# Optimization experiments

Hardware: AMD Instinct MI355X
Metric: run time of the kernel (lower is better)

Reference implementation:

```python
import jax, jax.numpy as jnp
import numpy as np


def _kernelize(data, projection_matrix):
    # FAVOR+ positive softmax features: ratio * h(x) * f(x @ P^T)
    # h(x) = exp(-||x||^2 / 2), f(u) = exp(u)
    d = data.shape[-1]
    r = projection_matrix.shape[0]
    data_norm = (d ** -0.25) * data                       # [n, d]
    ratio = r ** -0.5
    data_dash = jnp.einsum('id,rd->ir', data_norm, projection_matrix)  # [n, r]
    h = jnp.exp(-0.5 * jnp.sum(data_norm * data_norm, axis=-1, keepdims=True))  # [n, 1]
    return ratio * h * jnp.exp(data_dash)                 # [n, r]


def setup_inputs() -> dict:
    key = jax.random.key(0)
    k1, k2, k3, k4 = jax.random.split(key, 4)
    n, d, dv, r = 65536, 64, 64, 256
    q = jax.random.normal(k1, (n, d), dtype=jnp.float32)
    k = jax.random.normal(k2, (n, d), dtype=jnp.float32)
    v = jax.random.normal(k3, (n, dv), dtype=jnp.float32)
    projection_matrix = jax.random.normal(k4, (r, d), dtype=jnp.float32)
    return {"q": q, "k": k, "v": v, "projection_matrix": projection_matrix}


def reference(q, k, v, projection_matrix):
    q_hat = _kernelize(q, projection_matrix)              # [n, r]
    k_hat = _kernelize(k, projection_matrix)              # [n, r]
    z = k_hat.T @ v                                       # [r, dv]  (FAVOR associativity)
    w = q_hat @ z                                         # [n, dv]
    d_inv = 1.0 / jnp.sum(q_hat * jnp.sum(k_hat, axis=0), axis=1, keepdims=True)  # [n, 1]
    return d_inv * w
```

## Files before the change

kernel.cpp:

```cpp
#include <hip/hip_runtime.h>
#include <math.h>

typedef __attribute__((ext_vector_type(8))) short bf16x8;
typedef __attribute__((ext_vector_type(4))) float f32x4;

#define RFEAT 256
#define NBKV 512
#define LDK 136
#define PCOL 66
#define PARTU (128 * PCOL)
#define NGRP 8

#define SCLOG2E 0.51006971688f
#define RC_COEF -0.09016844006f
#define LOG2RATIO -4.0f

__device__ __forceinline__ unsigned short f2bf(float f) {
    union { float f; unsigned int u; } v; v.f = f;
    unsigned int r = v.u + 0x7FFFu + ((v.u >> 16) & 1u);
    return (unsigned short)(r >> 16);
}
__device__ __forceinline__ unsigned int pack2bf(float lo, float hi) {
    return (unsigned int)f2bf(lo) | ((unsigned int)f2bf(hi) << 16);
}
__device__ __forceinline__ float bf2f(unsigned int bits16) {
    union { unsigned int u; float f; } v; v.u = bits16 << 16; return v.f;
}

__global__ __launch_bounds__(256)
void prep_pb_kernel(const float* __restrict__ P, unsigned short* __restrict__ Pb)
{
    const int t = threadIdx.x, l = t & 63, g = t >> 6;
    for (int f = g * 8; f < g * 8 + 8; f++) {
        const int kstep = f >> 4, nt = f & 15;
        const float* src = P + (nt * 16 + (l & 15)) * 64 + kstep * 32 + (l >> 4) * 8;
        bf16x8 frag;
        #pragma unroll
        for (int j = 0; j < 8; j++) frag[j] = (short)f2bf(SCLOG2E * src[j]);
        *(bf16x8*)(Pb + f * 512 + l * 8) = frag;
    }
}

__device__ __forceinline__ void phi_chunk8(const float* __restrict__ X, int chunkBase,
                                           const unsigned short* __restrict__ Pb,
                                           unsigned short* phi_lds, float* rc)
{
    const int t = threadIdx.x, l = t & 63, w = t >> 6;
    if (t < 128) {
        const float4* xr = (const float4*)(X + (size_t)(chunkBase + t) * 64);
        float s0 = 0.f, s1 = 0.f;
        #pragma unroll
        for (int j = 0; j < 16; j += 2) {
            float4 a = xr[j];     s0 += a.x*a.x + a.y*a.y + a.z*a.z + a.w*a.w;
            float4 b = xr[j + 1]; s1 += b.x*b.x + b.y*b.y + b.z*b.z + b.w*b.w;
        }
        rc[t] = RC_COEF * (s0 + s1) + LOG2RATIO;
    }
    const float* ar = X + (size_t)(chunkBase + 16 * w + (l & 15)) * 64 + (l >> 4) * 8;
    bf16x8 a0, a1;
    #pragma unroll
    for (int j = 0; j < 8; j++) a0[j] = (short)f2bf(ar[j]);
    #pragma unroll
    for (int j = 0; j < 8; j++) a1[j] = (short)f2bf(ar[32 + j]);
    __syncthreads();
    const float4 rcv = *(const float4*)(rc + 16 * w + 4 * (l >> 4));
    #pragma unroll
    for (int nt = 0; nt < 16; nt++) {
        bf16x8 b0 = *(const bf16x8*)(Pb + nt * 512 + l * 8);
        bf16x8 b1 = *(const bf16x8*)(Pb + (16 + nt) * 512 + l * 8);
        f32x4 acc = (f32x4){rcv.x, rcv.y, rcv.z, rcv.w};
        acc = __builtin_amdgcn_mfma_f32_16x16x32_bf16(a0, b0, acc, 0, 0, 0);
        acc = __builtin_amdgcn_mfma_f32_16x16x32_bf16(a1, b1, acc, 0, 0, 0);
        float p0 = __builtin_amdgcn_exp2f(acc[0]);
        float p1 = __builtin_amdgcn_exp2f(acc[1]);
        float p2 = __builtin_amdgcn_exp2f(acc[2]);
        float p3 = __builtin_amdgcn_exp2f(acc[3]);
        const int col = nt * 16 + (l & 15);
        unsigned int w0 = pack2bf(p0, p1);
        unsigned int w1 = pack2bf(p2, p3);
        unsigned int* dst = (unsigned int*)(phi_lds + col * LDK + 16 * w + 4 * (l >> 4));
        dst[0] = w0;
        dst[1] = w1;
    }
    __syncthreads();
}

__global__ __launch_bounds__(512, 4)
void kv_kernel(const float* __restrict__ Kp, const float* __restrict__ V,
               const unsigned short* __restrict__ Pb, unsigned int* __restrict__ partials)
{
    __shared__ __align__(16) unsigned short phi_lds[RFEAT * LDK];
    __shared__ __align__(16) float rc[128];
    const int t = threadIdx.x, l = t & 63, w = t >> 6;

    f32x4 acc[2][5];
    #pragma unroll
    for (int mt = 0; mt < 2; mt++)
        #pragma unroll
        for (int nt = 0; nt < 5; nt++) acc[mt][nt] = (f32x4){0.f, 0.f, 0.f, 0.f};

    bf16x8 ones;
    #pragma unroll
    for (int j = 0; j < 8; j++) ones[j] = (short)(((l & 15) == 0) ? 0x3F80 : 0);

    const int cb = blockIdx.x * 128;
    phi_chunk8(Kp, cb, Pb, phi_lds, rc);

    #pragma unroll
    for (int ks = 0; ks < 4; ks++) {
        bf16x8 af[2];
        #pragma unroll
        for (int mt = 0; mt < 2; mt++)
            af[mt] = *(const bf16x8*)(phi_lds + (32 * w + mt * 16 + (l & 15)) * LDK
                                      + ks * 32 + (l >> 4) * 8);
        const float* vbase = V + (size_t)(cb + ks * 32 + (l >> 4) * 8) * 64 + (l & 15);
        bf16x8 bf4[4];
        #pragma unroll
        for (int nt = 0; nt < 4; nt++) {
            const float* vp = vbase + nt * 16;
            bf16x8 bb;
            #pragma unroll
            for (int j = 0; j < 8; j++) bb[j] = (short)f2bf(vp[j * 64]);
            bf4[nt] = bb;
        }
        #pragma unroll
        for (int mt = 0; mt < 2; mt++) {
            #pragma unroll
            for (int nt = 0; nt < 4; nt++)
                acc[mt][nt] = __builtin_amdgcn_mfma_f32_16x16x32_bf16(af[mt], bf4[nt], acc[mt][nt], 0, 0, 0);
            acc[mt][4] = __builtin_amdgcn_mfma_f32_16x16x32_bf16(af[mt], ones, acc[mt][4], 0, 0, 0);
        }
    }
    unsigned int* slot = partials + (size_t)blockIdx.x * PARTU;
    #pragma unroll
    for (int mt = 0; mt < 2; mt++) {
        const int fpb = 16 * w + mt * 8 + ((l >> 4) << 1);
        #pragma unroll
        for (int nt = 0; nt < 5; nt++) {
            if (nt == 4 && (l & 15) != 0) continue;
            const int col = nt * 16 + (l & 15);
            slot[fpb * PCOL + col]       = pack2bf(acc[mt][nt][0], acc[mt][nt][1]);
            slot[(fpb + 1) * PCOL + col] = pack2bf(acc[mt][nt][2], acc[mt][nt][3]);
        }
    }
}

__global__ __launch_bounds__(256)
void reduceA_kernel(const unsigned int* __restrict__ partials, float2* __restrict__ p2)
{
    const int idx = blockIdx.x * 256 + threadIdx.x;
    const int g = blockIdx.y;
    const unsigned int* base = partials + (size_t)g * 64 * PARTU + idx;
    float lo0 = 0.f, hi0 = 0.f, lo1 = 0.f, hi1 = 0.f;
    #pragma unroll 4
    for (int s = 0; s < 64; s += 2) {
        unsigned int u0 = base[(size_t)s * PARTU];
        unsigned int u1 = base[(size_t)(s + 1) * PARTU];
        lo0 += bf2f(u0 & 0xFFFFu); hi0 += bf2f(u0 >> 16);
        lo1 += bf2f(u1 & 0xFFFFu); hi1 += bf2f(u1 >> 16);
    }
    p2[(size_t)g * PARTU + idx] = make_float2(lo0 + lo1, hi0 + hi1);
}

__global__ __launch_bounds__(256)
void reduceB_kernel(const float2* __restrict__ p2, unsigned short* __restrict__ Zb)
{
    const int idx = blockIdx.x * 256 + threadIdx.x;
    float sLo = 0.f, sHi = 0.f;
    #pragma unroll
    for (int g = 0; g < NGRP; g++) {
        float2 v = p2[(size_t)g * PARTU + idx];
        sLo += v.x; sHi += v.y;
    }
    const int fp = idx / PCOL, col = idx - fp * PCOL;
    if (col >= 65) return;
    const int m0 = 2 * fp, m1 = m0 + 1;
    Zb[((m0 >> 3) * 80 + col) * 8 + (m0 & 7)] = f2bf(sLo);
    Zb[((m1 >> 3) * 80 + col) * 8 + (m1 & 7)] = f2bf(sHi);
}

__device__ __forceinline__ void phi_chunk_q(const float* __restrict__ X, int chunkBase,
                                            const unsigned short* __restrict__ Pb,
                                            unsigned short* phi_lds, float* rc)
{
    const int t = threadIdx.x, l = t & 63, w = t >> 6;
    if (t < 64) {
        const float4* xr = (const float4*)(X + (size_t)(chunkBase + t) * 64);
        float s0 = 0.f, s1 = 0.f;
        #pragma unroll
        for (int j = 0; j < 16; j += 2) {
            float4 a = xr[j];     s0 += a.x*a.x + a.y*a.y + a.z*a.z + a.w*a.w;
            float4 b = xr[j + 1]; s1 += b.x*b.x + b.y*b.y + b.z*b.z + b.w*b.w;
        }
        rc[t] = RC_COEF * (s0 + s1) + LOG2RATIO;
    }
    const float* ar = X + (size_t)(chunkBase + 16 * w + (l & 15)) * 64 + (l >> 4) * 8;
    bf16x8 a0, a1;
    #pragma unroll
    for (int j = 0; j < 8; j++) a0[j] = (short)f2bf(ar[j]);
    #pragma unroll
    for (int j = 0; j < 8; j++) a1[j] = (short)f2bf(ar[32 + j]);
    __syncthreads();
    const float4 rcv = *(const float4*)(rc + 16 * w + 4 * (l >> 4));
    #pragma unroll
    for (int nt = 0; nt < 16; nt++) {
        bf16x8 b0 = *(const bf16x8*)(Pb + nt * 512 + l * 8);
        bf16x8 b1 = *(const bf16x8*)(Pb + (16 + nt) * 512 + l * 8);
        f32x4 acc = (f32x4){rcv.x, rcv.y, rcv.z, rcv.w};
        acc = __builtin_amdgcn_mfma_f32_16x16x32_bf16(a0, b0, acc, 0, 0, 0);
        acc = __builtin_amdgcn_mfma_f32_16x16x32_bf16(a1, b1, acc, 0, 0, 0);
        float p0 = __builtin_amdgcn_exp2f(acc[0]);
        float p1 = __builtin_amdgcn_exp2f(acc[1]);
        float p2 = __builtin_amdgcn_exp2f(acc[2]);
        float p3 = __builtin_amdgcn_exp2f(acc[3]);
        const int col = nt * 16 + (l & 15);
        unsigned int w0 = pack2bf(p0, p1);
        unsigned int w1 = pack2bf(p2, p3);
        const int rb = (16 * w + (l >> 4) * 4) * 272 + col;
        phi_lds[rb]         = (unsigned short)(w0);
        phi_lds[rb + 272]   = (unsigned short)(w0 >> 16);
        phi_lds[rb + 544]   = (unsigned short)(w1);
        phi_lds[rb + 816]   = (unsigned short)(w1 >> 16);
    }
    __syncthreads();
}

__global__ __launch_bounds__(256, 4)
void q_out_kernel(const float* __restrict__ Q, const unsigned short* __restrict__ Pb,
                  const unsigned short* __restrict__ Zb, float* __restrict__ out)
{
    __shared__ __align__(16) unsigned short phi_lds[64 * 272];
    __shared__ __align__(16) float rc[64];
    const int t = threadIdx.x, l = t & 63, w = t >> 6;
    const int base = blockIdx.x * 64;

    phi_chunk_q(Q, base, Pb, phi_lds, rc);

    f32x4 acc[5];
    #pragma unroll
    for (int nt = 0; nt < 5; nt++) acc[nt] = (f32x4){0.f, 0.f, 0.f, 0.f};

    #pragma unroll
    for (int ks = 0; ks < 8; ks++) {
        bf16x8 a = *(const bf16x8*)(phi_lds + (16 * w + (l & 15)) * 272 + ks * 32 + (l >> 4) * 8);
        #pragma unroll
        for (int nt = 0; nt < 5; nt++) {
            bf16x8 b = *(const bf16x8*)(Zb + ((ks * 4 + (l >> 4)) * 80 + nt * 16 + (l & 15)) * 8);
            acc[nt] = __builtin_amdgcn_mfma_f32_16x16x32_bf16(a, b, acc[nt], 0, 0, 0);
        }
    }
    float inv[4];
    #pragma unroll
    for (int reg = 0; reg < 4; reg++) {
        float den = __shfl(acc[4][reg], (l & 48));
        inv[reg] = 1.0f / den;
    }
    const int row = base + 16 * w + (l >> 4) * 4;
    #pragma unroll
    for (int nt = 0; nt < 4; nt++)
        #pragma unroll
        for (int reg = 0; reg < 4; reg++)
            out[(size_t)(row + reg) * 64 + nt * 16 + (l & 15)] = acc[nt][reg] * inv[reg];
}

extern "C" void kernel_launch(void* const* d_in, const int* in_sizes, int n_in,
                              void* d_out, int out_size, void* d_ws, size_t ws_size,
                              hipStream_t stream) {
    const float* q = (const float*)d_in[0];
    const float* k = (const float*)d_in[1];
    const float* v = (const float*)d_in[2];
    const float* P = (const float*)d_in[3];
    float* out = (float*)d_out;

    unsigned short* Pb = (unsigned short*)d_ws;
    unsigned short* Zb = Pb + 32 * 512;
    float2* p2 = (float2*)((char*)d_ws + 73728);
    unsigned int* partials = (unsigned int*)((char*)d_ws + 73728 + 540672);

    prep_pb_kernel<<<1, 256, 0, stream>>>(P, Pb);
    kv_kernel<<<NBKV, 512, 0, stream>>>(k, v, Pb, partials);
    reduceA_kernel<<<dim3(33, NGRP), 256, 0, stream>>>(partials, p2);
    reduceB_kernel<<<33, 256, 0, stream>>>(p2, Zb);
    q_out_kernel<<<1024, 256, 0, stream>>>(q, Pb, Zb, out);
}
```

Before: 129.3 us.

## Stage V through XOR-swizzled LDS and swizzle phi layout in kv kernel

The phi tile in LDS drops its padded stride (LDK=136) for an XOR-swizzled 128-wide layout to avoid bank conflicts without padding. V is now loaded with coalesced per-thread row reads before the phi computation, converted to bf16 and transposed into a swizzled LDS buffer. The MFMA B fragments then come from LDS as vector loads instead of each wave doing strided scalar global loads per k-step. The rc scratch aliases the V LDS buffer, so correctness depends on the barrier inside phi_chunk8_swz ordering rc use before V is written. The early V loads also add sixteen registers per thread.

```diff
diff --git a/kernel.cpp b/kernel.cpp
--- a/kernel.cpp
+++ b/kernel.cpp
@@ -6,10 +6,12 @@
 
 #define RFEAT 256
 #define NBKV 512
-#define LDK 136
 #define PCOL 66
 #define PARTU (128 * PCOL)
 #define NGRP 8
+
+#define PHI_OFF(feat, row) ((feat) * 128 + ((row) ^ (((feat) & 7) << 3)))
+#define V_OFF(col, krow)   ((col) * 128 + ((krow) ^ (((col) & 7) << 3)))
 
 #define SCLOG2E 0.51006971688f
 #define RC_COEF -0.09016844006f
@@ -41,9 +43,9 @@
     }
 }
 
-__device__ __forceinline__ void phi_chunk8(const float* __restrict__ X, int chunkBase,
-                                           const unsigned short* __restrict__ Pb,
-                                           unsigned short* phi_lds, float* rc)
+__device__ __forceinline__ void phi_chunk8_swz(const float* __restrict__ X, int chunkBase,
+                                               const unsigned short* __restrict__ Pb,
+                                               unsigned short* phi_lds, float* rc)
 {
     const int t = threadIdx.x, l = t & 63, w = t >> 6;
     if (t < 128) {
@@ -76,11 +78,10 @@
         float p2 = __builtin_amdgcn_exp2f(acc[2]);
         float p3 = __builtin_amdgcn_exp2f(acc[3]);
         const int col = nt * 16 + (l & 15);
-        unsigned int w0 = pack2bf(p0, p1);
-        unsigned int w1 = pack2bf(p2, p3);
-        unsigned int* dst = (unsigned int*)(phi_lds + col * LDK + 16 * w + 4 * (l >> 4));
-        dst[0] = w0;
-        dst[1] = w1;
+        const int r0 = 16 * w + 4 * (l >> 4);
+        unsigned int* dst = (unsigned int*)(phi_lds + PHI_OFF(col, r0));
+        dst[0] = pack2bf(p0, p1);
+        dst[1] = pack2bf(p2, p3);
     }
     __syncthreads();
 }
@@ -89,9 +90,30 @@
 void kv_kernel(const float* __restrict__ Kp, const float* __restrict__ V,
                const unsigned short* __restrict__ Pb, unsigned int* __restrict__ partials)
 {
-    __shared__ __align__(16) unsigned short phi_lds[RFEAT * LDK];
-    __shared__ __align__(16) float rc[128];
-    const int t = threadIdx.x, l = t & 63, w = t >> 6;
+    __shared__ __align__(16) unsigned short phi_lds[RFEAT * 128];
+    __shared__ __align__(16) unsigned short v_lds[64 * 128];
+    float* rc = (float*)v_lds;
+    const int t = threadIdx.x, l = t & 63, w = t >> 6;
+    const int cb = blockIdx.x * 128;
+
+    const int vcol = t & 63, vr0 = (t >> 6) * 16;
+    float vreg[16];
+    #pragma unroll
+    for (int i = 0; i < 16; i++)
+        vreg[i] = V[(size_t)(cb + vr0 + i) * 64 + vcol];
+
+    phi_chunk8_swz(Kp, cb, Pb, phi_lds, rc);
+
+    {
+        unsigned int pk[8];
+        #pragma unroll
+        for (int i = 0; i < 8; i++) pk[i] = pack2bf(vreg[2 * i], vreg[2 * i + 1]);
+        unsigned int* d0 = (unsigned int*)(v_lds + V_OFF(vcol, vr0));
+        unsigned int* d1 = (unsigned int*)(v_lds + V_OFF(vcol, vr0 + 8));
+        d0[0] = pk[0]; d0[1] = pk[1]; d0[2] = pk[2]; d0[3] = pk[3];
+        d1[0] = pk[4]; d1[1] = pk[5]; d1[2] = pk[6]; d1[3] = pk[7];
+    }
+    __syncthreads();
 
     f32x4 acc[2][5];
     #pragma unroll
@@ -103,26 +125,17 @@
     #pragma unroll
     for (int j = 0; j < 8; j++) ones[j] = (short)(((l & 15) == 0) ? 0x3F80 : 0);
 
-    const int cb = blockIdx.x * 128;
-    phi_chunk8(Kp, cb, Pb, phi_lds, rc);
-
     #pragma unroll
     for (int ks = 0; ks < 4; ks++) {
+        const int krow0 = ks * 32 + (l >> 4) * 8;
         bf16x8 af[2];
         #pragma unroll
         for (int mt = 0; mt < 2; mt++)
-            af[mt] = *(const bf16x8*)(phi_lds + (32 * w + mt * 16 + (l & 15)) * LDK
-                                      + ks * 32 + (l >> 4) * 8);
-        const float* vbase = V + (size_t)(cb + ks * 32 + (l >> 4) * 8) * 64 + (l & 15);
+            af[mt] = *(const bf16x8*)(phi_lds + PHI_OFF(32 * w + mt * 16 + (l & 15), krow0));
         bf16x8 bf4[4];
         #pragma unroll
-        for (int nt = 0; nt < 4; nt++) {
-            const float* vp = vbase + nt * 16;
-            bf16x8 bb;
-            #pragma unroll
-            for (int j = 0; j < 8; j++) bb[j] = (short)f2bf(vp[j * 64]);
-            bf4[nt] = bb;
-        }
+        for (int nt = 0; nt < 4; nt++)
+            bf4[nt] = *(const bf16x8*)(v_lds + V_OFF(nt * 16 + (l & 15), krow0));
         #pragma unroll
         for (int mt = 0; mt < 2; mt++) {
             #pragma unroll
```

Result: no change. 128.0 us (-1.0%).
